# Kernel tuning notes

Measured on AMD Instinct MI355X. Metric: run time of the kernel, lower is better.

## Reference

```python
import jax, jax.numpy as jnp
import numpy as np

N, E, F_IN, H, C, G, NCLS, L = 50000, 600000, 128, 4, 64, 64, 3, 3
HC = H * C  # 256


def gatv2_layer(x, src, dst, Wl, bl, Wr, br, att, bias):
    # PyG GATv2Conv (concat=True, negative_slope=0.2, share_weights=False),
    # eval mode so attention dropout is identity.
    n = x.shape[0]
    xl = (x @ Wl + bl).reshape(n, H, C)  # source transform
    xr = (x @ Wr + br).reshape(n, H, C)  # target transform
    e = jax.nn.leaky_relu(xl[src] + xr[dst], negative_slope=0.2)  # [E',H,C]
    score = jnp.einsum('ehc,hc->eh', e, att)                      # [E',H]
    # softmax over incoming edges of each destination node
    mx = jax.ops.segment_max(score, dst, num_segments=n)
    ex = jnp.exp(score - mx[dst])
    denom = jax.ops.segment_sum(ex, dst, num_segments=n)
    alpha = ex / denom[dst]                                       # [E',H]
    out = jax.ops.segment_sum(alpha[..., None] * xl[src], dst, num_segments=n)
    return out.reshape(n, HC) + bias


def setup_inputs() -> dict:
    key = jax.random.key(0)
    ks = jax.random.split(key, 32)
    d = {}
    d['x'] = jax.random.normal(ks[0], (N, F_IN), dtype=jnp.float32)
    d['edge_index'] = jax.random.randint(ks[1], (2, E), 0, N, dtype=jnp.int64)
    d['batch'] = jnp.sort(jax.random.randint(ks[2], (N,), 0, G, dtype=jnp.int64))
    k = 3
    for li in range(L):
        fin = F_IN if li == 0 else HC
        s = 1.0 / np.sqrt(fin)
        d[f'Wl{li}'] = jax.random.normal(ks[k], (fin, HC), dtype=jnp.float32) * s; k += 1
        d[f'bl{li}'] = jnp.zeros((HC,), dtype=jnp.float32)
        d[f'Wr{li}'] = jax.random.normal(ks[k], (fin, HC), dtype=jnp.float32) * s; k += 1
        d[f'br{li}'] = jnp.zeros((HC,), dtype=jnp.float32)
        d[f'att{li}'] = jax.random.normal(ks[k], (H, C), dtype=jnp.float32) * (1.0 / np.sqrt(C)); k += 1
        d[f'bias{li}'] = jnp.zeros((HC,), dtype=jnp.float32)
    d['Wout'] = jax.random.normal(ks[k], (HC, NCLS), dtype=jnp.float32) * (1.0 / np.sqrt(HC))
    d['bout'] = jnp.zeros((NCLS,), dtype=jnp.float32)
    return d


def reference(x, edge_index, batch,
              Wl0, bl0, Wr0, br0, att0, bias0,
              Wl1, bl1, Wr1, br1, att1, bias1,
              Wl2, bl2, Wr2, br2, att2, bias2,
              Wout, bout):
    # add self loops (add_self_loops=True)
    loops = jnp.arange(N, dtype=edge_index.dtype)
    src = jnp.concatenate([edge_index[0], loops])
    dst = jnp.concatenate([edge_index[1], loops])

    h = gatv2_layer(x, src, dst, Wl0, bl0, Wr0, br0, att0, bias0)
    for (Wl, bl, Wr, br, att, bias) in [(Wl1, bl1, Wr1, br1, att1, bias1),
                                        (Wl2, bl2, Wr2, br2, att2, bias2)]:
        h = jax.nn.relu(h)
        h = gatv2_layer(h, src, dst, Wl, bl, Wr, br, att, bias)

    # pooling=0: mean + max over graphs
    counts = jax.ops.segment_sum(jnp.ones((N,), dtype=h.dtype), batch, num_segments=G)
    mean_p = jax.ops.segment_sum(h, batch, num_segments=G) / jnp.maximum(counts, 1.0)[:, None]
    max_p = jax.ops.segment_max(h, batch, num_segments=G)
    p = mean_p + max_p
    # dropout is identity in eval mode
    logits = p @ Wout + bout
    return jax.nn.softmax(logits, axis=1)
```

## Files before the change

kernel.cpp:

```cpp
#include <hip/hip_runtime.h>
#include <math.h>

#define N_NODES 50000
#define N_EDGES 600000
#define F_INPUT 128
#define HCDIM 256
#define NGRAPH 64
#define NCLS 3
#define MPAD 50048
#define SCAN_NB ((N_NODES + 255) / 256)
#define LOG2E 1.4426950408889634f
#define NPART 32

#define SPLITX_NB (MPAD * F_INPUT / 4 / 256)
#define ZERO_NB   (((MPAD - N_NODES) * HCDIM / 4 + 255) / 256)
#define WPREP_NB  (512 * (F_INPUT + HCDIM + HCDIM) / 256)
#define PREP_NB   (SPLITX_NB + ZERO_NB + WPREP_NB)
#define HIST_NB   ((N_EDGES + N_NODES + 255) / 256)
#define BND_NB    ((N_NODES + 255) / 256)

typedef float f32x4 __attribute__((ext_vector_type(4)));
typedef float f32x2 __attribute__((ext_vector_type(2)));
typedef _Float16 f16x8 __attribute__((ext_vector_type(8)));
typedef _Float16 f16x4 __attribute__((ext_vector_type(4)));
typedef _Float16 h2 __attribute__((ext_vector_type(2)));

__device__ __forceinline__ void gl_lds16(const void* g, void* l) {
    __builtin_amdgcn_global_load_lds(
        (const __attribute__((address_space(1))) unsigned int*)g,
        (__attribute__((address_space(3))) unsigned int*)l, 16, 0, 0);
}

__device__ __forceinline__ h2 bch2(unsigned int u) { return __builtin_bit_cast(h2, u); }
__device__ __forceinline__ h2 pk16(float a, float b) {
    return __builtin_bit_cast(h2, __builtin_amdgcn_cvt_pkrtz(a, b));
}

__device__ __forceinline__ h2 lrelu2(h2 v) {
    const h2 z = {(_Float16)0.f, (_Float16)0.f};
    const h2 c = {(_Float16)0.2f, (_Float16)0.2f};
    h2 mx = __builtin_elementwise_max(v, z);
    h2 mn = __builtin_elementwise_min(v, z);
    return mx + mn * c;
}

__global__ void hist_boundary_kernel(const int* __restrict__ ei, int* __restrict__ deg,
                                     const int* __restrict__ batch,
                                     int* __restrict__ startg, int* __restrict__ endg) {
    int b = blockIdx.x;
    if (b < HIST_NB) {
        int i = b * 256 + threadIdx.x;
        int total = N_EDGES + N_NODES;
        if (i >= total) return;
        int d = (i < N_EDGES) ? ei[N_EDGES + i] : (i - N_EDGES);
        atomicAdd(&deg[d], 1);
    } else {
        int i = (b - HIST_NB) * 256 + threadIdx.x;
        if (i >= N_NODES) return;
        int g = batch[i];
        if (i == 0 || batch[i - 1] != g) startg[g] = i;
        if (i == N_NODES - 1 || batch[i + 1] != g) endg[g] = i + 1;
    }
}

__global__ void block_scan_kernel(const int* __restrict__ deg, int* __restrict__ rowptr,
                                  int* __restrict__ bsums) {
    __shared__ int wt[4];
    int b = blockIdx.x, t = threadIdx.x, lane = t & 63, wid = t >> 6;
    int i = b * 256 + t;
    int v = (i < N_NODES) ? deg[i] : 0;
    int x = v;
    #pragma unroll
    for (int off = 1; off < 64; off <<= 1) {
        int y = __shfl_up(x, off, 64);
        if (lane >= off) x += y;
    }
    if (lane == 63) wt[wid] = x;
    __syncthreads();
    if (t == 0) {
        int s = 0;
        #pragma unroll
        for (int j = 0; j < 4; ++j) { int tv = wt[j]; wt[j] = s; s += tv; }
        bsums[b] = s;
    }
    __syncthreads();
    if (i < N_NODES) rowptr[i] = wt[wid] + x - v;
}

__global__ void add_off_kernel(int* __restrict__ rowptr, int* __restrict__ cursor,
                               const int* __restrict__ bsums) {
    __shared__ int red[256];
    int b = blockIdx.x, t = threadIdx.x;
    red[t] = (t < b) ? bsums[t] : 0;
    __syncthreads();
    for (int off = 128; off > 0; off >>= 1) {
        if (t < off) red[t] += red[t + off];
        __syncthreads();
    }
    int offv = red[0];
    int i = b * 256 + t;
    if (i < N_NODES) {
        int r = rowptr[i] + offv;
        rowptr[i] = r;
        cursor[i] = r;
    }
    if (i == 0) rowptr[N_NODES] = N_EDGES + N_NODES;
}

__global__ void fill_kernel(const int* __restrict__ ei, int* __restrict__ cursor,
                            int* __restrict__ colx) {
    int i = blockIdx.x * 256 + threadIdx.x;
    int total = N_EDGES + N_NODES;
    if (i >= total + 8) return;
    if (i >= total) { colx[i] = 0; return; }
    int s, d;
    if (i < N_EDGES) { s = ei[i]; d = ei[N_EDGES + i]; }
    else             { s = i - N_EDGES; d = s; }
    int pos = atomicAdd(&cursor[d], 1);
    colx[pos] = s * HCDIM;
}

__global__ void prep_kernel(const float* __restrict__ x, _Float16* __restrict__ A,
                            _Float16* __restrict__ Bt0, _Float16* __restrict__ Bt1,
                            _Float16* __restrict__ Bt2,
                            const float* __restrict__ Wl0, const float* __restrict__ Wr0,
                            const float* __restrict__ Wl1, const float* __restrict__ Wr1,
                            const float* __restrict__ Wl2, const float* __restrict__ Wr2) {
    int b = blockIdx.x;
    if (b < SPLITX_NB) {
        int base = (b * 256 + threadIdx.x) * 4;
        int row = base >> 7;
        float4 v = make_float4(0.f, 0.f, 0.f, 0.f);
        if (row < N_NODES) v = *(const float4*)&x[base];
        f16x4 o;
        o.x = (_Float16)v.x; o.y = (_Float16)v.y; o.z = (_Float16)v.z; o.w = (_Float16)v.w;
        *(f16x4*)&A[base] = o;
    } else if (b < SPLITX_NB + ZERO_NB) {
        int i = ((b - SPLITX_NB) * 256 + threadIdx.x) * 4;
        if (i < (MPAD - N_NODES) * HCDIM) {
            f16x4 z = {(_Float16)0.f, (_Float16)0.f, (_Float16)0.f, (_Float16)0.f};
            *(f16x4*)&A[(size_t)N_NODES * HCDIM + i] = z;
        }
    } else {
        int t = (b - SPLITX_NB - ZERO_NB) * 256 + threadIdx.x;
        const float* Wl; const float* Wr; _Float16* Bt; int K;
        if (t < 512 * F_INPUT)            { Wl = Wl0; Wr = Wr0; Bt = Bt0; K = F_INPUT; }
        else if (t < 512 * (F_INPUT + HCDIM)) { t -= 512 * F_INPUT; Wl = Wl1; Wr = Wr1; Bt = Bt1; K = HCDIM; }
        else                              { t -= 512 * (F_INPUT + HCDIM); Wl = Wl2; Wr = Wr2; Bt = Bt2; K = HCDIM; }
        int n = t & 511, k = t >> 9;
        float w = (n < 256) ? Wl[k * 256 + n] : Wr[k * 256 + (n - 256)];
        Bt[n * K + k] = (_Float16)w;
    }
}

__global__ __launch_bounds__(256) void gemm_mfma(
    const _Float16* __restrict__ A, const _Float16* __restrict__ B,
    int K,
    const float* __restrict__ bl, const float* __restrict__ br,
    unsigned char* __restrict__ xl8, _Float16* __restrict__ xrh)
{
    __shared__ _Float16 sA[64 * 64], sB[128 * 64];
    int tid = threadIdx.x;
    int lane = tid & 63, wave = tid >> 6;
    int wm = wave >> 1, wn = wave & 1;
    int bx = blockIdx.x >> 2, by = blockIdx.x & 3;
    int row0 = bx * 64;
    int n0 = by * 128;
    int quad = lane >> 4, l16 = lane & 15;

    f32x4 acc[2][4];
    #pragma unroll
    for (int i = 0; i < 2; ++i)
        #pragma unroll
        for (int j = 0; j < 4; ++j)
            acc[i][j] = (f32x4){0.f, 0.f, 0.f, 0.f};

    for (int k0 = 0; k0 < K; k0 += 64) {
        __syncthreads();
        #pragma unroll
        for (int pass = 0; pass < 2; ++pass) {
            int c = tid + pass * 256;
            int r = c >> 3;
            int pl = c & 7;
            int pg = pl ^ (r & 7);
            size_t ga = (size_t)(row0 + r) * K + k0 + pg * 8;
            gl_lds16(A + ga, sA + c * 8);
        }
        #pragma unroll
        for (int pass = 0; pass < 4; ++pass) {
            int c = tid + pass * 256;
            int r = c >> 3;
            int pl = c & 7;
            int pg = pl ^ (r & 7);
            size_t gb = (size_t)(n0 + r) * K + k0 + pg * 8;
            gl_lds16(B + gb, sB + c * 8);
        }
        __syncthreads();

        #pragma unroll
        for (int kk = 0; kk < 2; ++kk) {
            f16x8 fa[2], fb[4];
            #pragma unroll
            for (int i = 0; i < 2; ++i) {
                int rr = wm * 32 + i * 16 + l16;
                int ca = (kk * 4 + quad) ^ (rr & 7);
                fa[i] = *(const f16x8*)&sA[rr * 64 + ca * 8];
            }
            #pragma unroll
            for (int j = 0; j < 4; ++j) {
                int nn = wn * 64 + j * 16 + l16;
                int cb = (kk * 4 + quad) ^ (nn & 7);
                fb[j] = *(const f16x8*)&sB[nn * 64 + cb * 8];
            }
            #pragma unroll
            for (int i = 0; i < 2; ++i)
                #pragma unroll
                for (int j = 0; j < 4; ++j)
                    acc[i][j] = __builtin_amdgcn_mfma_f32_16x16x32_f16(fa[i], fb[j], acc[i][j], 0, 0, 0);
        }
    }

    if (by < 2) {
        int cb0 = by * 128;
        #pragma unroll
        for (int j = 0; j < 4; ++j) {
            int col = cb0 + wn * 64 + j * 16 + l16;
            float bj = bl[col];
            #pragma unroll
            for (int i = 0; i < 2; ++i) {
                int rbase = row0 + wm * 32 + i * 16 + quad * 4;
                #pragma unroll
                for (int r = 0; r < 4; ++r) {
                    int row = rbase + r;
                    if (row < N_NODES) {
                        float v = acc[i][j][r] + bj;
                        int pk = __builtin_amdgcn_cvt_pk_fp8_f32(v, v, 0, false);
                        xl8[(size_t)row * HCDIM + col] = (unsigned char)pk;
                    }
                }
            }
        }
    } else {
        int cb0 = (by - 2) * 128;
        #pragma unroll
        for (int j = 0; j < 4; ++j) {
            int col = cb0 + wn * 64 + j * 16 + l16;
            float bj = br[col];
            #pragma unroll
            for (int i = 0; i < 2; ++i) {
                int rbase = row0 + wm * 32 + i * 16 + quad * 4;
                #pragma unroll
                for (int r = 0; r < 4; ++r) {
                    int row = rbase + r;
                    if (row < N_NODES)
                        xrh[(size_t)row * HCDIM + col] = (_Float16)(acc[i][j][r] + bj);
                }
            }
        }
    }
}

__global__ __launch_bounds__(256) void gat_edge(
    const unsigned char* __restrict__ xl8, const _Float16* __restrict__ xrh,
    const float* __restrict__ att, const float* __restrict__ bias,
    const int* __restrict__ rowptr, const int* __restrict__ colx,
    _Float16* __restrict__ outh, _Float16* __restrict__ onext, int mode)
{
    int wave = threadIdx.x >> 6;
    int lane = threadIdx.x & 63;
    int q  = lane >> 4;
    int ql = lane & 15;
    int node = blockIdx.x * 4 + wave;
    if (node >= N_NODES) return;
    int cb = ql * 16;

    const char* xrrow = (const char*)xrh + (size_t)node * (HCDIM * 2) + cb * 2;
    uint4 xu0 = *(const uint4*)xrrow;
    uint4 xu1 = *(const uint4*)(xrrow + 16);
    h2 xr[8] = { bch2(xu0.x), bch2(xu0.y), bch2(xu0.z), bch2(xu0.w),
                 bch2(xu1.x), bch2(xu1.y), bch2(xu1.z), bch2(xu1.w) };
    h2 at[8];
    #pragma unroll
    for (int i = 0; i < 8; ++i) {
        float2 av = *(const float2*)&att[cb + i * 2];
        at[i] = (h2){(_Float16)(av.x * LOG2E), (_Float16)(av.y * LOG2E)};
    }

    int e0 = rowptr[node], e1 = rowptr[node + 1];
    float denom = 0.f;
    float acc[16];
    #pragma unroll
    for (int i = 0; i < 16; ++i) acc[i] = 0.f;

    uint4 d = *(const uint4*)(xl8 + (unsigned)(colx[e0 + q] + cb));

    for (int e = e0; e < e1; e += 4) {
        uint4 nd = *(const uint4*)(xl8 + (unsigned)(colx[e + 4 + q] + cb));

        unsigned int dw[4] = {d.x, d.y, d.z, d.w};
        f32x2 flo[4], fhi[4];
        h2 hx[8];
        #pragma unroll
        for (int j = 0; j < 4; ++j) {
            flo[j] = __builtin_amdgcn_cvt_pk_f32_fp8(dw[j], false);
            fhi[j] = __builtin_amdgcn_cvt_pk_f32_fp8(dw[j], true);
            hx[2 * j]     = pk16(flo[j].x, flo[j].y);
            hx[2 * j + 1] = pk16(fhi[j].x, fhi[j].y);
        }
        float pa = 0.f, pb = 0.f;
        #pragma unroll
        for (int i = 0; i < 4; ++i) {
            pa = __builtin_amdgcn_fdot2(lrelu2(hx[i] + xr[i]), at[i], pa, false);
            pb = __builtin_amdgcn_fdot2(lrelu2(hx[i + 4] + xr[i + 4]), at[i + 4], pb, false);
        }
        float p = pa + pb;
        p += __builtin_bit_cast(float, __builtin_amdgcn_ds_swizzle(__builtin_bit_cast(int, p), 0x041F));
        p += __builtin_bit_cast(float, __builtin_amdgcn_ds_swizzle(__builtin_bit_cast(int, p), 0x081F));

        float w;
        if (e + 4 <= e1) {
            w = exp2f(p);
        } else {
            w = (e + q < e1) ? exp2f(p) : 0.f;
        }
        denom += w;
        #pragma unroll
        for (int j = 0; j < 4; ++j) {
            acc[4 * j]     += w * flo[j].x;
            acc[4 * j + 1] += w * flo[j].y;
            acc[4 * j + 2] += w * fhi[j].x;
            acc[4 * j + 3] += w * fhi[j].y;
        }
        d = nd;
    }

    denom += __shfl_xor(denom, 16, 64);
    denom += __shfl_xor(denom, 32, 64);
    #pragma unroll
    for (int i = 0; i < 16; ++i) {
        acc[i] += __shfl_xor(acc[i], 16, 64);
        acc[i] += __shfl_xor(acc[i], 32, 64);
    }

    if (q == 0) {
        float inv = 1.f / denom;
        char* orow = (char*)(mode == 0 ? outh : onext) + (size_t)node * (HCDIM * 2) + cb * 2;
        h2 o[8];
        #pragma unroll
        for (int i = 0; i < 8; ++i) {
            float2 bv = *(const float2*)&bias[cb + i * 2];
            float v0 = acc[2 * i] * inv + bv.x;
            float v1 = acc[2 * i + 1] * inv + bv.y;
            if (mode != 0) { v0 = fmaxf(v0, 0.f); v1 = fmaxf(v1, 0.f); }
            o[i] = pk16(v0, v1);
        }
        uint4 s0 = { __builtin_bit_cast(unsigned int, o[0]), __builtin_bit_cast(unsigned int, o[1]),
                     __builtin_bit_cast(unsigned int, o[2]), __builtin_bit_cast(unsigned int, o[3]) };
        uint4 s1 = { __builtin_bit_cast(unsigned int, o[4]), __builtin_bit_cast(unsigned int, o[5]),
                     __builtin_bit_cast(unsigned int, o[6]), __builtin_bit_cast(unsigned int, o[7]) };
        *(uint4*)orow = s0;
        *(uint4*)(orow + 16) = s1;
    }
}

__global__ __launch_bounds__(256) void pool_partial(
    const _Float16* __restrict__ h, const int* __restrict__ startg,
    const int* __restrict__ endg, float* __restrict__ sumP, float* __restrict__ maxP)
{
    __shared__ float4 sS[4][64];
    __shared__ float4 sM[4][64];
    int g = blockIdx.x >> 5, part = blockIdx.x & (NPART - 1);
    int lane = threadIdx.x & 63;
    int sub = threadIdx.x >> 6;
    int c0 = lane * 4;
    int s = startg[g], e = endg[g];
    float4 sum = make_float4(0.f, 0.f, 0.f, 0.f);
    float4 mx = make_float4(-INFINITY, -INFINITY, -INFINITY, -INFINITY);
    for (int i = s + part * 4 + sub; i < e; i += NPART * 4) {
        uint2 u = *(const uint2*)&h[(size_t)i * HCDIM + c0];
        h2 a = bch2(u.x), b = bch2(u.y);
        float4 v = make_float4((float)a.x, (float)a.y, (float)b.x, (float)b.y);
        sum.x += v.x; sum.y += v.y; sum.z += v.z; sum.w += v.w;
        mx.x = fmaxf(mx.x, v.x); mx.y = fmaxf(mx.y, v.y);
        mx.z = fmaxf(mx.z, v.z); mx.w = fmaxf(mx.w, v.w);
    }
    sS[sub][lane] = sum; sM[sub][lane] = mx;
    __syncthreads();
    if (sub == 0) {
        #pragma unroll
        for (int j = 1; j < 4; ++j) {
            float4 a = sS[j][lane], b = sM[j][lane];
            sum.x += a.x; sum.y += a.y; sum.z += a.z; sum.w += a.w;
            mx.x = fmaxf(mx.x, b.x); mx.y = fmaxf(mx.y, b.y);
            mx.z = fmaxf(mx.z, b.z); mx.w = fmaxf(mx.w, b.w);
        }
        size_t o = (size_t)blockIdx.x * HCDIM + c0;
        *(float4*)&sumP[o] = sum;
        *(float4*)&maxP[o] = mx;
    }
}

__global__ __launch_bounds__(256) void pool_final_logits(
    const float* __restrict__ sumP, const float* __restrict__ maxP,
    const int* __restrict__ startg, const int* __restrict__ endg,
    const float* __restrict__ Wout, const float* __restrict__ bout,
    float* __restrict__ out)
{
    __shared__ float red[256];
    __shared__ float lg[NCLS];
    int g = blockIdx.x, c = threadIdx.x;
    float s = 0.f, m = -INFINITY;
    #pragma unroll 8
    for (int part = 0; part < NPART; ++part) {
        size_t o = (size_t)(g * NPART + part) * HCDIM + c;
        s += sumP[o];
        m = fmaxf(m, maxP[o]);
    }
    int cnt = endg[g] - startg[g];
    float inv = 1.f / fmaxf((float)cnt, 1.f);
    float pv = s * inv + m;

    for (int j = 0; j < NCLS; ++j) {
        red[c] = pv * Wout[c * NCLS + j];
        __syncthreads();
        for (int off = 128; off > 0; off >>= 1) {
            if (c < off) red[c] += red[c + off];
            __syncthreads();
        }
        if (c == 0) lg[j] = red[0] + bout[j];
        __syncthreads();
    }
    if (c == 0) {
        float mx = fmaxf(lg[0], fmaxf(lg[1], lg[2]));
        float e0 = __expf(lg[0] - mx), e1 = __expf(lg[1] - mx), e2 = __expf(lg[2] - mx);
        float invs = 1.f / (e0 + e1 + e2);
        out[g * NCLS + 0] = e0 * invs;
        out[g * NCLS + 1] = e1 * invs;
        out[g * NCLS + 2] = e2 * invs;
    }
}

extern "C" void kernel_launch(void* const* d_in, const int* in_sizes, int n_in,
                              void* d_out, int out_size, void* d_ws, size_t ws_size,
                              hipStream_t stream) {
    const float* x     = (const float*)d_in[0];
    const int*   ei    = (const int*)d_in[1];
    const int*   batch = (const int*)d_in[2];
    const float *Wl[3], *bl[3], *Wr[3], *br[3], *att[3], *bias[3];
    for (int li = 0; li < 3; ++li) {
        int b = 3 + li * 6;
        Wl[li]   = (const float*)d_in[b + 0];
        bl[li]   = (const float*)d_in[b + 1];
        Wr[li]   = (const float*)d_in[b + 2];
        br[li]   = (const float*)d_in[b + 3];
        att[li]  = (const float*)d_in[b + 4];
        bias[li] = (const float*)d_in[b + 5];
    }
    const float* Wout = (const float*)d_in[21];
    const float* bout = (const float*)d_in[22];
    float* out = (float*)d_out;

    size_t off = 0;
    char* wsb = (char*)d_ws;
    auto alloc = [&](size_t bytes) -> char* {
        char* ptr = wsb + off;
        off += (bytes + 255) & ~(size_t)255;
        return ptr;
    };
    int* zblk    = (int*)alloc((N_NODES + 2 * NGRAPH) * sizeof(int));
    int* deg     = zblk;
    int* startg  = zblk + N_NODES;
    int* endg    = zblk + N_NODES + NGRAPH;
    int* rowptr  = (int*)alloc((N_NODES + 1) * sizeof(int));
    int* cursor  = (int*)alloc(N_NODES * sizeof(int));
    int* bsums   = (int*)alloc(256 * sizeof(int));
    int* colx    = (int*)alloc((size_t)(N_EDGES + N_NODES + 8) * sizeof(int));
    _Float16* Abuf = (_Float16*)alloc((size_t)MPAD * HCDIM * sizeof(_Float16));
    _Float16* Bt[3];
    for (int li = 0; li < 3; ++li) {
        int K = (li == 0) ? F_INPUT : HCDIM;
        Bt[li] = (_Float16*)alloc((size_t)512 * K * sizeof(_Float16));
    }
    unsigned char* xl8 = (unsigned char*)alloc((size_t)N_NODES * HCDIM);
    _Float16* xrh  = (_Float16*)alloc((size_t)N_NODES * HCDIM * sizeof(_Float16));
    _Float16* hbuf = (_Float16*)alloc((size_t)N_NODES * HCDIM * sizeof(_Float16));
    float* sumP    = (float*)alloc((size_t)NGRAPH * NPART * HCDIM * sizeof(float));
    float* maxP    = (float*)alloc((size_t)NGRAPH * NPART * HCDIM * sizeof(float));

    hipMemsetAsync(zblk, 0, (N_NODES + 2 * NGRAPH) * sizeof(int), stream);

    hist_boundary_kernel<<<HIST_NB + BND_NB, 256, 0, stream>>>(ei, deg, batch, startg, endg);
    block_scan_kernel<<<SCAN_NB, 256, 0, stream>>>(deg, rowptr, bsums);
    add_off_kernel<<<SCAN_NB, 256, 0, stream>>>(rowptr, cursor, bsums);
    fill_kernel<<<(N_EDGES + N_NODES + 8 + 255) / 256, 256, 0, stream>>>(ei, cursor, colx);

    prep_kernel<<<PREP_NB, 256, 0, stream>>>(x, Abuf, Bt[0], Bt[1], Bt[2],
                                             Wl[0], Wr[0], Wl[1], Wr[1], Wl[2], Wr[2]);

    for (int li = 0; li < 3; ++li) {
        int K = (li == 0) ? F_INPUT : HCDIM;
        gemm_mfma<<<(MPAD / 64) * 4, 256, 0, stream>>>(
            Abuf, Bt[li], K, bl[li], br[li], xl8, xrh);
        if (li < 2) {
            gat_edge<<<N_NODES / 4, 256, 0, stream>>>(
                xl8, xrh, att[li], bias[li], rowptr, colx, nullptr, Abuf, 1);
        } else {
            gat_edge<<<N_NODES / 4, 256, 0, stream>>>(
                xl8, xrh, att[li], bias[li], rowptr, colx, hbuf, nullptr, 0);
        }
    }

    pool_partial<<<NGRAPH * NPART, 256, 0, stream>>>(hbuf, startg, endg, sumP, maxP);
    pool_final_logits<<<NGRAPH, 256, 0, stream>>>(sumP, maxP, startg, endg, Wout, bout, out);
}
```

Baseline: 452.6 us.

## Unroll GAT edge loop by two groups with deeper gather prefetch

Result: slower. 462.9 us (+2.3%).

```diff
diff --git a/kernel.cpp b/kernel.cpp
--- a/kernel.cpp
+++ b/kernel.cpp
@@ -11,6 +11,7 @@
 #define SCAN_NB ((N_NODES + 255) / 256)
 #define LOG2E 1.4426950408889634f
 #define NPART 32
+#define COLX_PAD 16
 
 #define SPLITX_NB (MPAD * F_INPUT / 4 / 256)
 #define ZERO_NB   (((MPAD - N_NODES) * HCDIM / 4 + 255) / 256)
@@ -34,14 +35,6 @@
 __device__ __forceinline__ h2 bch2(unsigned int u) { return __builtin_bit_cast(h2, u); }
 __device__ __forceinline__ h2 pk16(float a, float b) {
     return __builtin_bit_cast(h2, __builtin_amdgcn_cvt_pkrtz(a, b));
-}
-
-__device__ __forceinline__ h2 lrelu2(h2 v) {
-    const h2 z = {(_Float16)0.f, (_Float16)0.f};
-    const h2 c = {(_Float16)0.2f, (_Float16)0.2f};
-    h2 mx = __builtin_elementwise_max(v, z);
-    h2 mn = __builtin_elementwise_min(v, z);
-    return mx + mn * c;
 }
 
 __global__ void hist_boundary_kernel(const int* __restrict__ ei, int* __restrict__ deg,
@@ -111,7 +104,7 @@
                             int* __restrict__ colx) {
     int i = blockIdx.x * 256 + threadIdx.x;
     int total = N_EDGES + N_NODES;
-    if (i >= total + 8) return;
+    if (i >= total + COLX_PAD) return;
     if (i >= total) { colx[i] = 0; return; }
     int s, d;
     if (i < N_EDGES) { s = ei[i]; d = ei[N_EDGES + i]; }
@@ -288,58 +281,79 @@
 
     int e0 = rowptr[node], e1 = rowptr[node + 1];
     float denom = 0.f;
-    float acc[16];
+    f32x2 accp[8];
     #pragma unroll
-    for (int i = 0; i < 16; ++i) acc[i] = 0.f;
-
-    uint4 d = *(const uint4*)(xl8 + (unsigned)(colx[e0 + q] + cb));
-
-    for (int e = e0; e < e1; e += 4) {
-        uint4 nd = *(const uint4*)(xl8 + (unsigned)(colx[e + 4 + q] + cb));
-
-        unsigned int dw[4] = {d.x, d.y, d.z, d.w};
-        f32x2 flo[4], fhi[4];
+    for (int i = 0; i < 8; ++i) accp[i] = (f32x2){0.f, 0.f};
+
+    const unsigned char* xb = xl8 + cb;
+    const h2 slope = {(_Float16)0.2f, (_Float16)0.2f};
+
+    int cx0 = colx[e0 + q];
+    int cx1 = colx[e0 + 4 + q];
+    uint4 d0 = *(const uint4*)(xb + (unsigned)cx0);
+    uint4 d1 = *(const uint4*)(xb + (unsigned)cx1);
+    cx0 = colx[e0 + 8 + q];
+    cx1 = colx[e0 + 12 + q];
+
+    auto process = [&](uint4 dd, int ebase, bool masked) {
+        unsigned int dw[4] = {dd.x, dd.y, dd.z, dd.w};
+        f32x2 lo[4], hi[4];
         h2 hx[8];
         #pragma unroll
         for (int j = 0; j < 4; ++j) {
-            flo[j] = __builtin_amdgcn_cvt_pk_f32_fp8(dw[j], false);
-            fhi[j] = __builtin_amdgcn_cvt_pk_f32_fp8(dw[j], true);
-            hx[2 * j]     = pk16(flo[j].x, flo[j].y);
-            hx[2 * j + 1] = pk16(fhi[j].x, fhi[j].y);
+            lo[j] = __builtin_amdgcn_cvt_pk_f32_fp8(dw[j], false);
+            hi[j] = __builtin_amdgcn_cvt_pk_f32_fp8(dw[j], true);
+            hx[2 * j]     = pk16(lo[j].x, lo[j].y);
+            hx[2 * j + 1] = pk16(hi[j].x, hi[j].y);
         }
         float pa = 0.f, pb = 0.f;
         #pragma unroll
         for (int i = 0; i < 4; ++i) {
-            pa = __builtin_amdgcn_fdot2(lrelu2(hx[i] + xr[i]), at[i], pa, false);
-            pb = __builtin_amdgcn_fdot2(lrelu2(hx[i + 4] + xr[i + 4]), at[i + 4], pb, false);
+            h2 va = hx[i] + xr[i];
+            h2 vb = hx[i + 4] + xr[i + 4];
+            va = __builtin_elementwise_max(va, va * slope);
+            vb = __builtin_elementwise_max(vb, vb * slope);
+            pa = __builtin_amdgcn_fdot2(va, at[i], pa, false);
+            pb = __builtin_amdgcn_fdot2(vb, at[i + 4], pb, false);
         }
         float p = pa + pb;
         p += __builtin_bit_cast(float, __builtin_amdgcn_ds_swizzle(__builtin_bit_cast(int, p), 0x041F));
         p += __builtin_bit_cast(float, __builtin_amdgcn_ds_swizzle(__builtin_bit_cast(int, p), 0x081F));
-
-        float w;
-        if (e + 4 <= e1) {
-            w = exp2f(p);
-        } else {
-            w = (e + q < e1) ? exp2f(p) : 0.f;
-        }
+        float w = exp2f(p);
+        if (masked) w = (ebase + q < e1) ? w : 0.f;
         denom += w;
+        f32x2 wp = {w, w};
         #pragma unroll
         for (int j = 0; j < 4; ++j) {
-            acc[4 * j]     += w * flo[j].x;
-            acc[4 * j + 1] += w * flo[j].y;
-            acc[4 * j + 2] += w * fhi[j].x;
-            acc[4 * j + 3] += w * fhi[j].y;
-        }
-        d = nd;
+            accp[2 * j]     += wp * lo[j];
+            accp[2 * j + 1] += wp * hi[j];
+        }
+    };
+
+    int e = e0;
+    for (; e + 8 <= e1; e += 8) {
+        uint4 n0 = *(const uint4*)(xb + (unsigned)cx0);
+        uint4 n1 = *(const uint4*)(xb + (unsigned)cx1);
+        cx0 = colx[e + 16 + q];
+        cx1 = colx[e + 20 + q];
+        process(d0, e, false);
+        process(d1, e + 4, false);
+        d0 = n0; d1 = n1;
+    }
+    if (e < e1) {
+        process(d0, e, true);
+        e += 4;
+        if (e < e1) process(d1, e, true);
     }
 
     denom += __shfl_xor(denom, 16, 64);
     denom += __shfl_xor(denom, 32, 64);
     #pragma unroll
-    for (int i = 0; i < 16; ++i) {
-        acc[i] += __shfl_xor(acc[i], 16, 64);
-        acc[i] += __shfl_xor(acc[i], 32, 64);
+    for (int i = 0; i < 8; ++i) {
+        accp[i].x += __shfl_xor(accp[i].x, 16, 64);
+        accp[i].x += __shfl_xor(accp[i].x, 32, 64);
+        accp[i].y += __shfl_xor(accp[i].y, 16, 64);
+        accp[i].y += __shfl_xor(accp[i].y, 32, 64);
     }
 
     if (q == 0) {
@@ -349,8 +363,8 @@
         #pragma unroll
         for (int i = 0; i < 8; ++i) {
             float2 bv = *(const float2*)&bias[cb + i * 2];
-            float v0 = acc[2 * i] * inv + bv.x;
-            float v1 = acc[2 * i + 1] * inv + bv.y;
+            float v0 = accp[i].x * inv + bv.x;
+            float v1 = accp[i].y * inv + bv.y;
             if (mode != 0) { v0 = fmaxf(v0, 0.f); v1 = fmaxf(v1, 0.f); }
             o[i] = pk16(v0, v1);
         }
@@ -474,7 +488,7 @@
     int* rowptr  = (int*)alloc((N_NODES + 1) * sizeof(int));
     int* cursor  = (int*)alloc(N_NODES * sizeof(int));
     int* bsums   = (int*)alloc(256 * sizeof(int));
-    int* colx    = (int*)alloc((size_t)(N_EDGES + N_NODES + 8) * sizeof(int));
+    int* colx    = (int*)alloc((size_t)(N_EDGES + N_NODES + COLX_PAD) * sizeof(int));
     _Float16* Abuf = (_Float16*)alloc((size_t)MPAD * HCDIM * sizeof(_Float16));
     _Float16* Bt[3];
     for (int li = 0; li < 3; ++li) {
@@ -492,7 +506,7 @@
     hist_boundary_kernel<<<HIST_NB + BND_NB, 256, 0, stream>>>(ei, deg, batch, startg, endg);
     block_scan_kernel<<<SCAN_NB, 256, 0, stream>>>(deg, rowptr, bsums);
     add_off_kernel<<<SCAN_NB, 256, 0, stream>>>(rowptr, cursor, bsums);
-    fill_kernel<<<(N_EDGES + N_NODES + 8 + 255) / 256, 256, 0, stream>>>(ei, cursor, colx);
+    fill_kernel<<<(N_EDGES + N_NODES + COLX_PAD + 255) / 256, 256, 0, stream>>>(ei, cursor, colx);
 
     prep_kernel<<<PREP_NB, 256, 0, stream>>>(x, Abuf, Bt[0], Bt[1], Bt[2],
                                              Wl[0], Wr[0], Wl[1], Wr[1], Wl[2], Wr[2]);
```
